# Kernel tuning notes

Measured on AMD Instinct MI355X. Metric: run time of the kernel, lower is better.

The kernel has to match this reference:

```python
import jax, jax.numpy as jnp
import numpy as np

N = 8192          # number of priors
TOP_K = 50        # max detections returned
IOU_THR = 0.3     # NMS IoU threshold (module-level constant)
VAR0, VAR1 = 0.1, 0.2  # variance buffer


def setup_inputs() -> dict:
    key = jax.random.key(0)
    k1, k2, k3, k4, k5 = jax.random.split(key, 5)
    loc = jax.random.normal(k1, (N, 14), jnp.float32)
    conf = jax.random.uniform(k2, (N, 2), jnp.float32)
    # some iou scores slightly out of [0,1] to exercise the clamp
    iou = jax.random.uniform(k3, (N, 1), jnp.float32) * 1.2 - 0.1
    cxcy = jax.random.uniform(k4, (N, 2), jnp.float32)            # anchor centers in [0,1)
    wh = jax.random.uniform(k5, (N, 2), jnp.float32) * 0.19 + 0.01  # anchor sizes in (0.01,0.2)
    priors = jnp.concatenate([cxcy, wh], axis=1)
    return {"loc": loc, "conf": conf, "iou": iou, "priors": priors}


def _decode(loc, conf, iou, priors):
    cls_scores = conf[:, 1]
    iou_scores = jnp.clip(iou[:, 0], 0.0, 1.0)
    scores = jnp.sqrt(cls_scores * iou_scores)
    p_cxcy, p_wh = priors[:, 0:2], priors[:, 2:4]
    bb_cxcy = p_cxcy + loc[:, 0:2] * VAR0 * p_wh
    var = jnp.array([VAR0, VAR1], jnp.float32)
    bb_wh_half = p_wh * jnp.exp(loc[:, 2:4] * var) * 0.5
    bboxes = jnp.concatenate([bb_cxcy - bb_wh_half, bb_cxcy + bb_wh_half], axis=1)
    # 5 landmarks, each decoded like the box center
    lms = jnp.concatenate(
        [p_cxcy + loc[:, 4 + 2 * i:6 + 2 * i] * VAR0 * p_wh for i in range(5)], axis=1)
    return bboxes, lms, scores


def _nms_keep_idx(bboxes, scores):
    """Greedy NMS; returns indices (into original order) of the first TOP_K kept boxes."""
    order = jnp.argsort(-scores)
    b = bboxes[order]
    x1, y1, x2, y2 = b[:, 0], b[:, 1], b[:, 2], b[:, 3]
    area = (x2 - x1) * (y2 - y1)
    iw = jnp.maximum(jnp.minimum(x2[:, None], x2[None, :]) - jnp.maximum(x1[:, None], x1[None, :]), 0.0)
    ih = jnp.maximum(jnp.minimum(y2[:, None], y2[None, :]) - jnp.maximum(y1[:, None], y1[None, :]), 0.0)
    inter = iw * ih
    iou_mat = inter / (area[:, None] + area[None, :] - inter)  # [N, N]
    idxs = jnp.arange(N)

    def body(i, keep):
        suppressed = jnp.any((iou_mat[i] > IOU_THR) & keep & (idxs < i))
        return keep.at[i].set(~suppressed)

    keep = jax.lax.fori_loop(0, N, body, jnp.zeros((N,), bool))
    kept_pos = jnp.nonzero(keep, size=TOP_K, fill_value=0)[0]  # fixed-size under jit
    return order[kept_pos]


def reference(loc, conf, iou, priors):
    bboxes, lms, scores = _decode(loc, conf, iou, priors)
    keep_idx = _nms_keep_idx(bboxes, scores)
    dets = jnp.concatenate(
        [bboxes[keep_idx], lms[keep_idx], scores[keep_idx][:, None]], axis=1)  # [TOP_K, 15]
    return dets
```

## Files before the change

### kernel.cpp

```cpp
#include <hip/hip_runtime.h>

#define NBOX 8192
#define TOP_K 50
#define IOU_THR 0.3f
#define VAR0 0.1f
#define VAR1 0.2f
#define NT 512
#define NWAVE (NT / 64)
#define MSEL 128
#define CAND_MAX 1024
#define BPT 16

__device__ __forceinline__ void decode_box(int cidx, const float* __restrict__ loc,
                                           const float* __restrict__ priors,
                                           float& x1, float& y1, float& x2, float& y2,
                                           float& area)
{
    float4 pr = *reinterpret_cast<const float4*>(priors + 4 * cidx);
    float l0 = loc[cidx * 14 + 0];
    float l1 = loc[cidx * 14 + 1];
    float l2 = loc[cidx * 14 + 2];
    float l3 = loc[cidx * 14 + 3];
    float cx = pr.x + l0 * VAR0 * pr.z;
    float cy = pr.y + l1 * VAR0 * pr.w;
    float hw = pr.z * expf(l2 * VAR0) * 0.5f;
    float hh = pr.w * expf(l3 * VAR1) * 0.5f;
    x1 = cx - hw; y1 = cy - hh; x2 = cx + hw; y2 = cy + hh;
    area = (x2 - x1) * (y2 - y1);
}

__device__ __forceinline__ void find_thresh(unsigned c0, unsigned c1, unsigned c2, unsigned c3,
                                            unsigned base_above, int lane,
                                            int& bin_sel, unsigned& above_sel)
{
    unsigned cnt = c0 + c1 + c2 + c3;
    unsigned S = cnt;
    #pragma unroll
    for (int d = 1; d < 64; d <<= 1) {
        unsigned t = __shfl_down(S, d);
        if (lane + d < 64) S += t;
    }
    unsigned long long bal = __ballot(base_above + S >= MSEL);
    int lstar = 63 - __clzll(bal);
    int src = (lstar < 63) ? (lstar + 1) : lstar;
    unsigned Snext = __shfl(S, src);
    unsigned above = base_above + ((lstar < 63) ? Snext : 0u);
    unsigned bl[4] = {c0, c1, c2, c3};
    int bsel = -1; unsigned abv = above; unsigned acc = above;
    #pragma unroll
    for (int k = 3; k >= 0; --k) {
        if (bsel < 0) {
            if (acc + bl[k] >= MSEL) { bsel = k; abv = acc; }
            else acc += bl[k];
        }
    }
    bin_sel  = 4 * lstar + __shfl(bsel, lstar);
    above_sel = __shfl(abv, lstar);
}

__device__ void bitonic_sort(unsigned long long* a, int S, int tid)
{
    for (int k = 2; k <= S; k <<= 1) {
        for (int j = k >> 1; j > 0; j >>= 1) {
            __syncthreads();
            for (int i = tid; i < S; i += NT) {
                int l = i ^ j;
                if (l > i) {
                    unsigned long long A = a[i];
                    unsigned long long B = a[l];
                    bool asc = ((i & k) == 0);
                    if ((A > B) == asc) { a[i] = B; a[l] = A; }
                }
            }
        }
    }
    __syncthreads();
}

__device__ int greedy_nms_serial(const unsigned long long* __restrict__ arr, int n, int lane,
                                 const float* __restrict__ loc, const float* __restrict__ priors,
                                 int* keep_out)
{
    float kx1 = 0.f, ky1 = 0.f, kx2 = 0.f, ky2 = 0.f, karea = 0.f;
    int my_keep = 0, idx0 = 0, kept = 0;
    bool done = false;
    for (int p = 0; p < n && !done; p += 64) {
        int cidx = 0;
        float x1 = 0.f, y1 = 0.f, x2 = 0.f, y2 = 0.f, area = 0.f;
        int pos = p + lane;
        if (pos < n) {
            cidx = (int)(arr[pos] & 0xFFFFFFFFull);
            decode_box(cidx, loc, priors, x1, y1, x2, y2, area);
        }
        int nb = (n - p) < 64 ? (n - p) : 64;
        for (int c = 0; c < nb; ++c) {
            float bx1 = __shfl(x1, c);
            float by1 = __shfl(y1, c);
            float bx2 = __shfl(x2, c);
            float by2 = __shfl(y2, c);
            float barea = __shfl(area, c);
            int   bidx  = __shfl(cidx, c);
            float iw = fmaxf(fminf(kx2, bx2) - fmaxf(kx1, bx1), 0.0f);
            float ih = fmaxf(fminf(ky2, by2) - fmaxf(ky1, by1), 0.0f);
            float inter = iw * ih;
            float v = inter / (karea + barea - inter);
            bool sup = (lane < kept) && (v > IOU_THR);
            if (__ballot(sup) == 0ull) {
                if (kept == 0) idx0 = bidx;
                if (lane == kept) {
                    kx1 = bx1; ky1 = by1; kx2 = bx2; ky2 = by2; karea = barea;
                    my_keep = bidx;
                }
                ++kept;
                if (kept == TOP_K) { done = true; break; }
            }
        }
    }
    if (lane < TOP_K) keep_out[lane] = (lane < kept) ? my_keep : idx0;
    return kept;
}

__global__ __launch_bounds__(NT) void yunet_fused_kernel(
    const float* __restrict__ loc,
    const float* __restrict__ conf,
    const float* __restrict__ iou,
    const float* __restrict__ priors,
    float* __restrict__ out)
{
    __shared__ unsigned long long keys[NBOX];
    __shared__ unsigned long long cand[CAND_MAX];
    __shared__ unsigned int hist[NWAVE][256];
    __shared__ unsigned int fhist[256];
    __shared__ unsigned long long maskbuf[64];
    __shared__ unsigned long long sh_supprev;
    __shared__ float4 boxb4[64];
    __shared__ float  boxa[64];
    __shared__ float4 keptb4[TOP_K];
    __shared__ float  kepta[TOP_K];
    __shared__ int keep_sh[TOP_K];
    __shared__ unsigned sh_cnt, sh_above, sh_T;
    __shared__ int sh_B, sh_flag, sh_kept;

    const int tid = threadIdx.x;

    {
        unsigned* hz = &hist[0][0];
        for (int i = tid; i < NWAVE * 256; i += NT) hz[i] = 0;
        for (int i = tid; i < 256; i += NT) fhist[i] = 0;
        if (tid == 0) { sh_cnt = 0; sh_flag = 0; sh_kept = 0; }
    }
    __syncthreads();

    unsigned sbv[BPT];
    {
        const float4* conf4 = reinterpret_cast<const float4*>(conf);
        const float4* iou4  = reinterpret_cast<const float4*>(iou);
        float4 cf[8], io[4];
        #pragma unroll
        for (int m = 0; m < 2; ++m)
            #pragma unroll
            for (int q = 0; q < 4; ++q)
                cf[m * 4 + q] = conf4[(m * NT + tid) * 4 + q];
        #pragma unroll
        for (int m = 0; m < 2; ++m)
            #pragma unroll
            for (int r = 0; r < 2; ++r)
                io[m * 2 + r] = iou4[(m * NT + tid) * 2 + r];

        #pragma unroll
        for (int m = 0; m < 2; ++m) {
            float sc[8], uu[8];
            #pragma unroll
            for (int q = 0; q < 4; ++q) {
                sc[2 * q]     = cf[m * 4 + q].y;
                sc[2 * q + 1] = cf[m * 4 + q].w;
            }
            #pragma unroll
            for (int r = 0; r < 2; ++r) {
                uu[4 * r + 0] = io[m * 2 + r].x; uu[4 * r + 1] = io[m * 2 + r].y;
                uu[4 * r + 2] = io[m * 2 + r].z; uu[4 * r + 3] = io[m * 2 + r].w;
            }
            #pragma unroll
            for (int q = 0; q < 8; ++q) {
                float u = fminf(fmaxf(uu[q], 0.0f), 1.0f);
                float s = sqrtf(sc[q] * u);
                unsigned sb = __float_as_uint(s);
                sbv[m * 8 + q] = sb;
                atomicAdd(&hist[tid >> 6][sb >> 24], 1u);
            }
        }
    }
    __syncthreads();

    if (tid < 64) {
        const int lane = tid;
        unsigned c0 = 0, c1 = 0, c2 = 0, c3 = 0;
        #pragma unroll
        for (int w = 0; w < NWAVE; ++w) {
            c0 += hist[w][4 * lane + 0];
            c1 += hist[w][4 * lane + 1];
            c2 += hist[w][4 * lane + 2];
            c3 += hist[w][4 * lane + 3];
        }
        int bs; unsigned ab;
        find_thresh(c0, c1, c2, c3, 0u, lane, bs, ab);
        if (lane == 0) { sh_B = bs; sh_above = ab; }
    }
    __syncthreads();
    const int B = sh_B;
    const unsigned above = sh_above;

    #pragma unroll
    for (int k = 0; k < BPT; ++k) {
        unsigned sb = sbv[k];
        if ((int)(sb >> 24) == B) atomicAdd(&fhist[(sb >> 16) & 255u], 1u);
    }
    __syncthreads();

    if (tid < 64) {
        const int lane = tid;
        int fs; unsigned ab2;
        find_thresh(fhist[4 * lane + 0], fhist[4 * lane + 1],
                    fhist[4 * lane + 2], fhist[4 * lane + 3], above, lane, fs, ab2);
        if (lane == 0) sh_T = ((unsigned)B << 24) | ((unsigned)fs << 16);
    }
    __syncthreads();
    const unsigned T = sh_T;

    #pragma unroll
    for (int m = 0; m < 2; ++m) {
        #pragma unroll
        for (int q = 0; q < 8; ++q) {
            unsigned sb = sbv[m * 8 + q];
            if (sb >= T) {
                unsigned pos = atomicAdd(&sh_cnt, 1u);
                if (pos < CAND_MAX)
                    cand[pos] = ((unsigned long long)(~sb) << 32)
                              | (unsigned)((m * NT + tid) * BPT / 2 + q);
            }
        }
    }
    __syncthreads();
    const int C = (int)sh_cnt;

    if (C <= CAND_MAX) {
        for (int i = tid; i < C; i += NT) {
            unsigned long long k = cand[i];
            int r = 0;
            int j = 0;
            for (; j + 4 <= C; j += 4) {
                r += (cand[j]     < k) ? 1 : 0;
                r += (cand[j + 1] < k) ? 1 : 0;
                r += (cand[j + 2] < k) ? 1 : 0;
                r += (cand[j + 3] < k) ? 1 : 0;
            }
            for (; j < C; ++j) r += (cand[j] < k) ? 1 : 0;
            keys[r] = k;
        }
        __syncthreads();

        for (int p = 0; p < C; p += 64) {
            if (tid < 64) {
                const int lane = tid;
                int pos = p + lane;
                bool valid = pos < C;
                int cidx = valid ? (int)(keys[pos] & 0xFFFFFFFFull) : 0;
                float x1, y1, x2, y2, area;
                decode_box(cidx, loc, priors, x1, y1, x2, y2, area);
                boxb4[lane] = make_float4(x1, y1, x2, y2);
                boxa[lane] = area;
                int kept = sh_kept;
                bool supP = !valid;
                for (int j = 0; j < kept; ++j) {
                    float4 kb = keptb4[j]; float ka = kepta[j];
                    float iw = fmaxf(fminf(x2, kb.z) - fmaxf(x1, kb.x), 0.f);
                    float ih = fmaxf(fminf(y2, kb.w) - fmaxf(y1, kb.y), 0.f);
                    float inter = iw * ih;
                    supP = supP || (inter > IOU_THR * (area + ka - inter));
                }
                unsigned long long sp = __ballot(supP);
                if (lane == 0) sh_supprev = sp;
            }
            __syncthreads();

            {
                int r  = tid >> 3;
                int cb = tid & 7;
                float4 rb = boxb4[r]; float ra = boxa[r];
                unsigned byte = 0;
                #pragma unroll
                for (int k = 0; k < 8; ++k) {
                    int c = cb * 8 + k;
                    float4 cx = boxb4[c]; float ca = boxa[c];
                    float iw = fmaxf(fminf(rb.z, cx.z) - fmaxf(rb.x, cx.x), 0.f);
                    float ih = fmaxf(fminf(rb.w, cx.w) - fmaxf(rb.y, cx.y), 0.f);
                    float inter = iw * ih;
                    byte |= (unsigned)((inter > IOU_THR * (ra + ca - inter)) ? 1u : 0u) << k;
                }
                ((unsigned char*)maskbuf)[tid] = (unsigned char)byte;
            }
            __syncthreads();

            if (tid < 64) {
                const int lane = tid;
                unsigned long long mymask = maskbuf[lane];
                unsigned long long sup_prev = sh_supprev;
                unsigned long long keepcur = 0ull;
                for (int i2 = 0; i2 < 64; ++i2) {
                    unsigned long long mi = __shfl(mymask, i2);
                    unsigned long long lower = (i2 == 0) ? 0ull : (~0ull >> (64 - i2));
                    if (!((sup_prev >> i2) & 1ull) && !(mi & keepcur & lower))
                        keepcur |= (1ull << i2);
                }
                int kept = sh_kept;
                unsigned long long lowm = (lane == 0) ? 0ull : (~0ull >> (64 - lane));
                int rank = kept + __popcll(keepcur & lowm);
                if (((keepcur >> lane) & 1ull) && rank < TOP_K) {
                    keep_sh[rank] = (int)(keys[p + lane] & 0xFFFFFFFFull);
                    keptb4[rank] = boxb4[lane];
                    kepta[rank] = boxa[lane];
                }
                if (lane == 0) sh_kept = kept + __popcll(keepcur);
            }
            __syncthreads();
            if (sh_kept >= TOP_K) break;
        }
        if (tid == 0) sh_flag = (sh_kept >= TOP_K) ? 0 : 1;
    } else {
        if (tid == 0) sh_flag = 1;
    }
    __syncthreads();

    if (sh_flag) {
        #pragma unroll
        for (int m = 0; m < 2; ++m) {
            #pragma unroll
            for (int q = 0; q < 8; ++q) {
                int i = (m * NT + tid) * 8 + q;
                keys[i] = ((unsigned long long)(~sbv[m * 8 + q]) << 32) | (unsigned)i;
            }
        }
        __syncthreads();
        bitonic_sort(keys, NBOX, tid);
        if (tid < 64) greedy_nms_serial(keys, NBOX, tid, loc, priors, keep_sh);
        __syncthreads();
    }

    if (tid < TOP_K) {
        int i = keep_sh[tid];
        float4 pr = *reinterpret_cast<const float4*>(priors + 4 * i);
        float cx = pr.x + loc[i * 14 + 0] * VAR0 * pr.z;
        float cy = pr.y + loc[i * 14 + 1] * VAR0 * pr.w;
        float hw = pr.z * expf(loc[i * 14 + 2] * VAR0) * 0.5f;
        float hh = pr.w * expf(loc[i * 14 + 3] * VAR1) * 0.5f;
        float* o = out + tid * 15;
        o[0] = cx - hw;
        o[1] = cy - hh;
        o[2] = cx + hw;
        o[3] = cy + hh;
        #pragma unroll
        for (int q = 0; q < 5; ++q) {
            o[4 + 2 * q] = pr.x + loc[i * 14 + 4 + 2 * q] * VAR0 * pr.z;
            o[5 + 2 * q] = pr.y + loc[i * 14 + 5 + 2 * q] * VAR0 * pr.w;
        }
        float cc = conf[i * 2 + 1];
        float u  = fminf(fmaxf(iou[i], 0.0f), 1.0f);
        o[14] = sqrtf(cc * u);
    }
}

extern "C" void kernel_launch(void* const* d_in, const int* in_sizes, int n_in,
                              void* d_out, int out_size, void* d_ws, size_t ws_size,
                              hipStream_t stream) {
    const float* loc    = (const float*)d_in[0];
    const float* conf   = (const float*)d_in[1];
    const float* iou    = (const float*)d_in[2];
    const float* priors = (const float*)d_in[3];
    float* out = (float*)d_out;

    yunet_fused_kernel<<<1, NT, 0, stream>>>(loc, conf, iou, priors, out);
}
```

Baseline: 23.27 us.

## Use single-pass linear-bin score histogram and predecode candidate boxes in parallel

After: 23.18 us. Within noise of the previous version (-0.4%).

```diff
diff --git a/kernel.cpp b/kernel.cpp
--- a/kernel.cpp
+++ b/kernel.cpp
@@ -8,7 +8,7 @@
 #define NT 512
 #define NWAVE (NT / 64)
 #define MSEL 128
-#define CAND_MAX 1024
+#define PRE_MAX 256
 #define BPT 16
 
 __device__ __forceinline__ void decode_box(int cidx, const float* __restrict__ loc,
@@ -128,126 +128,102 @@
     float* __restrict__ out)
 {
     __shared__ unsigned long long keys[NBOX];
-    __shared__ unsigned long long cand[CAND_MAX];
-    __shared__ unsigned int hist[NWAVE][256];
-    __shared__ unsigned int fhist[256];
+    __shared__ unsigned long long cand[PRE_MAX];
+    __shared__ unsigned hist[NWAVE][256] __attribute__((aligned(16)));
     __shared__ unsigned long long maskbuf[64];
     __shared__ unsigned long long sh_supprev;
-    __shared__ float4 boxb4[64];
-    __shared__ float  boxa[64];
+    __shared__ float4 boxs4[PRE_MAX];
+    __shared__ float  boxsa[PRE_MAX];
     __shared__ float4 keptb4[TOP_K];
     __shared__ float  kepta[TOP_K];
     __shared__ int keep_sh[TOP_K];
-    __shared__ unsigned sh_cnt, sh_above, sh_T;
-    __shared__ int sh_B, sh_flag, sh_kept;
+    __shared__ unsigned sh_cnt;
+    __shared__ int sh_flag, sh_kept;
 
     const int tid = threadIdx.x;
+    const int lane = tid & 63;
+
+    const float4* conf4 = reinterpret_cast<const float4*>(conf);
+    const float4* iou4  = reinterpret_cast<const float4*>(iou);
+    float4 cf[8], io[4];
+    #pragma unroll
+    for (int m = 0; m < 2; ++m)
+        #pragma unroll
+        for (int q = 0; q < 4; ++q)
+            cf[m * 4 + q] = conf4[(m * NT + tid) * 4 + q];
+    #pragma unroll
+    for (int m = 0; m < 2; ++m)
+        #pragma unroll
+        for (int r = 0; r < 2; ++r)
+            io[m * 2 + r] = iou4[(m * NT + tid) * 2 + r];
 
     {
         unsigned* hz = &hist[0][0];
         for (int i = tid; i < NWAVE * 256; i += NT) hz[i] = 0;
-        for (int i = tid; i < 256; i += NT) fhist[i] = 0;
         if (tid == 0) { sh_cnt = 0; sh_flag = 0; sh_kept = 0; }
     }
     __syncthreads();
 
     unsigned sbv[BPT];
+    #pragma unroll
+    for (int m = 0; m < 2; ++m) {
+        float sc[8], uu[8];
+        #pragma unroll
+        for (int q = 0; q < 4; ++q) {
+            sc[2 * q]     = cf[m * 4 + q].y;
+            sc[2 * q + 1] = cf[m * 4 + q].w;
+        }
+        #pragma unroll
+        for (int r = 0; r < 2; ++r) {
+            uu[4 * r + 0] = io[m * 2 + r].x; uu[4 * r + 1] = io[m * 2 + r].y;
+            uu[4 * r + 2] = io[m * 2 + r].z; uu[4 * r + 3] = io[m * 2 + r].w;
+        }
+        #pragma unroll
+        for (int q = 0; q < 8; ++q) {
+            float u = fminf(fmaxf(uu[q], 0.0f), 1.0f);
+            float s = sqrtf(sc[q] * u);
+            unsigned sb = __float_as_uint(s);
+            sbv[m * 8 + q] = sb;
+            int bin = (int)(s * 256.0f); bin = bin > 255 ? 255 : bin;
+            atomicAdd(&hist[tid >> 6][bin], 1u);
+        }
+    }
+    __syncthreads();
+
+    int B;
     {
-        const float4* conf4 = reinterpret_cast<const float4*>(conf);
-        const float4* iou4  = reinterpret_cast<const float4*>(iou);
-        float4 cf[8], io[4];
-        #pragma unroll
-        for (int m = 0; m < 2; ++m)
-            #pragma unroll
-            for (int q = 0; q < 4; ++q)
-                cf[m * 4 + q] = conf4[(m * NT + tid) * 4 + q];
-        #pragma unroll
-        for (int m = 0; m < 2; ++m)
-            #pragma unroll
-            for (int r = 0; r < 2; ++r)
-                io[m * 2 + r] = iou4[(m * NT + tid) * 2 + r];
-
-        #pragma unroll
-        for (int m = 0; m < 2; ++m) {
-            float sc[8], uu[8];
-            #pragma unroll
-            for (int q = 0; q < 4; ++q) {
-                sc[2 * q]     = cf[m * 4 + q].y;
-                sc[2 * q + 1] = cf[m * 4 + q].w;
-            }
-            #pragma unroll
-            for (int r = 0; r < 2; ++r) {
-                uu[4 * r + 0] = io[m * 2 + r].x; uu[4 * r + 1] = io[m * 2 + r].y;
-                uu[4 * r + 2] = io[m * 2 + r].z; uu[4 * r + 3] = io[m * 2 + r].w;
-            }
-            #pragma unroll
-            for (int q = 0; q < 8; ++q) {
-                float u = fminf(fmaxf(uu[q], 0.0f), 1.0f);
-                float s = sqrtf(sc[q] * u);
-                unsigned sb = __float_as_uint(s);
-                sbv[m * 8 + q] = sb;
-                atomicAdd(&hist[tid >> 6][sb >> 24], 1u);
-            }
-        }
-    }
-    __syncthreads();
-
-    if (tid < 64) {
-        const int lane = tid;
         unsigned c0 = 0, c1 = 0, c2 = 0, c3 = 0;
         #pragma unroll
         for (int w = 0; w < NWAVE; ++w) {
-            c0 += hist[w][4 * lane + 0];
-            c1 += hist[w][4 * lane + 1];
-            c2 += hist[w][4 * lane + 2];
-            c3 += hist[w][4 * lane + 3];
-        }
-        int bs; unsigned ab;
-        find_thresh(c0, c1, c2, c3, 0u, lane, bs, ab);
-        if (lane == 0) { sh_B = bs; sh_above = ab; }
-    }
-    __syncthreads();
-    const int B = sh_B;
-    const unsigned above = sh_above;
-
-    #pragma unroll
-    for (int k = 0; k < BPT; ++k) {
-        unsigned sb = sbv[k];
-        if ((int)(sb >> 24) == B) atomicAdd(&fhist[(sb >> 16) & 255u], 1u);
-    }
-    __syncthreads();
-
-    if (tid < 64) {
-        const int lane = tid;
-        int fs; unsigned ab2;
-        find_thresh(fhist[4 * lane + 0], fhist[4 * lane + 1],
-                    fhist[4 * lane + 2], fhist[4 * lane + 3], above, lane, fs, ab2);
-        if (lane == 0) sh_T = ((unsigned)B << 24) | ((unsigned)fs << 16);
-    }
-    __syncthreads();
-    const unsigned T = sh_T;
+            uint4 h = *(const uint4*)&hist[w][4 * lane];
+            c0 += h.x; c1 += h.y; c2 += h.z; c3 += h.w;
+        }
+        unsigned ab;
+        find_thresh(c0, c1, c2, c3, 0u, lane, B, ab);
+    }
 
     #pragma unroll
     for (int m = 0; m < 2; ++m) {
         #pragma unroll
         for (int q = 0; q < 8; ++q) {
             unsigned sb = sbv[m * 8 + q];
-            if (sb >= T) {
+            float s = __uint_as_float(sb);
+            int bin = (int)(s * 256.0f); bin = bin > 255 ? 255 : bin;
+            if (bin >= B) {
                 unsigned pos = atomicAdd(&sh_cnt, 1u);
-                if (pos < CAND_MAX)
+                if (pos < PRE_MAX)
                     cand[pos] = ((unsigned long long)(~sb) << 32)
-                              | (unsigned)((m * NT + tid) * BPT / 2 + q);
+                              | (unsigned)((m * NT + tid) * 8 + q);
             }
         }
     }
     __syncthreads();
     const int C = (int)sh_cnt;
 
-    if (C <= CAND_MAX) {
-        for (int i = tid; i < C; i += NT) {
-            unsigned long long k = cand[i];
-            int r = 0;
-            int j = 0;
+    if (C <= PRE_MAX) {
+        if (tid < C) {
+            unsigned long long k = cand[tid];
+            int r = 0, j = 0;
             for (; j + 4 <= C; j += 4) {
                 r += (cand[j]     < k) ? 1 : 0;
                 r += (cand[j + 1] < k) ? 1 : 0;
@@ -256,27 +232,28 @@
             }
             for (; j < C; ++j) r += (cand[j] < k) ? 1 : 0;
             keys[r] = k;
+            int cidx = (int)(k & 0xFFFFFFFFull);
+            float x1, y1, x2, y2, area;
+            decode_box(cidx, loc, priors, x1, y1, x2, y2, area);
+            boxs4[r] = make_float4(x1, y1, x2, y2);
+            boxsa[r] = area;
         }
         __syncthreads();
 
         for (int p = 0; p < C; p += 64) {
             if (tid < 64) {
-                const int lane = tid;
                 int pos = p + lane;
                 bool valid = pos < C;
-                int cidx = valid ? (int)(keys[pos] & 0xFFFFFFFFull) : 0;
-                float x1, y1, x2, y2, area;
-                decode_box(cidx, loc, priors, x1, y1, x2, y2, area);
-                boxb4[lane] = make_float4(x1, y1, x2, y2);
-                boxa[lane] = area;
+                int rp = valid ? pos : 0;
+                float4 b = boxs4[rp]; float a = boxsa[rp];
                 int kept = sh_kept;
                 bool supP = !valid;
                 for (int j = 0; j < kept; ++j) {
                     float4 kb = keptb4[j]; float ka = kepta[j];
-                    float iw = fmaxf(fminf(x2, kb.z) - fmaxf(x1, kb.x), 0.f);
-                    float ih = fmaxf(fminf(y2, kb.w) - fmaxf(y1, kb.y), 0.f);
+                    float iw = fmaxf(fminf(b.z, kb.z) - fmaxf(b.x, kb.x), 0.f);
+                    float ih = fmaxf(fminf(b.w, kb.w) - fmaxf(b.y, kb.y), 0.f);
                     float inter = iw * ih;
-                    supP = supP || (inter > IOU_THR * (area + ka - inter));
+                    supP = supP || (inter > IOU_THR * (a + ka - inter));
                 }
                 unsigned long long sp = __ballot(supP);
                 if (lane == 0) sh_supprev = sp;
@@ -286,12 +263,14 @@
             {
                 int r  = tid >> 3;
                 int cb = tid & 7;
-                float4 rb = boxb4[r]; float ra = boxa[r];
+                int rp = (p + r < C) ? p + r : 0;
+                float4 rb = boxs4[rp]; float ra = boxsa[rp];
                 unsigned byte = 0;
                 #pragma unroll
                 for (int k = 0; k < 8; ++k) {
                     int c = cb * 8 + k;
-                    float4 cx = boxb4[c]; float ca = boxa[c];
+                    int cp = (p + c < C) ? p + c : 0;
+                    float4 cx = boxs4[cp]; float ca = boxsa[cp];
                     float iw = fmaxf(fminf(rb.z, cx.z) - fmaxf(rb.x, cx.x), 0.f);
                     float ih = fmaxf(fminf(rb.w, cx.w) - fmaxf(rb.y, cx.y), 0.f);
                     float inter = iw * ih;
@@ -302,25 +281,28 @@
             __syncthreads();
 
             if (tid < 64) {
-                const int lane = tid;
                 unsigned long long mymask = maskbuf[lane];
                 unsigned long long sup_prev = sh_supprev;
                 unsigned long long keepcur = 0ull;
-                for (int i2 = 0; i2 < 64; ++i2) {
+                const int kept0 = sh_kept;
+                int kept = kept0;
+                for (int i2 = 0; i2 < 64 && kept < TOP_K; ++i2) {
                     unsigned long long mi = __shfl(mymask, i2);
-                    unsigned long long lower = (i2 == 0) ? 0ull : (~0ull >> (64 - i2));
-                    if (!((sup_prev >> i2) & 1ull) && !(mi & keepcur & lower))
-                        keepcur |= (1ull << i2);
-                }
-                int kept = sh_kept;
-                unsigned long long lowm = (lane == 0) ? 0ull : (~0ull >> (64 - lane));
-                int rank = kept + __popcll(keepcur & lowm);
+                    unsigned long long lower = (1ull << i2) - 1ull;
+                    if (!((sup_prev >> i2) & 1ull) && !(mi & keepcur & lower)) {
+                        keepcur |= 1ull << i2;
+                        ++kept;
+                    }
+                }
+                unsigned long long lowm = (1ull << lane) - 1ull;
+                int rank = kept0 + __popcll(keepcur & lowm);
                 if (((keepcur >> lane) & 1ull) && rank < TOP_K) {
-                    keep_sh[rank] = (int)(keys[p + lane] & 0xFFFFFFFFull);
-                    keptb4[rank] = boxb4[lane];
-                    kepta[rank] = boxa[lane];
-                }
-                if (lane == 0) sh_kept = kept + __popcll(keepcur);
+                    int pos = p + lane;
+                    keep_sh[rank] = (int)(keys[pos] & 0xFFFFFFFFull);
+                    keptb4[rank] = boxs4[pos];
+                    kepta[rank] = boxsa[pos];
+                }
+                if (lane == 0) sh_kept = kept;
             }
             __syncthreads();
             if (sh_kept >= TOP_K) break;
@@ -343,11 +325,13 @@
         __syncthreads();
         bitonic_sort(keys, NBOX, tid);
         if (tid < 64) greedy_nms_serial(keys, NBOX, tid, loc, priors, keep_sh);
+        if (tid == 0) sh_kept = TOP_K;
         __syncthreads();
     }
 
     if (tid < TOP_K) {
-        int i = keep_sh[tid];
+        int src = (tid < sh_kept) ? tid : 0;
+        int i = keep_sh[src];
         float4 pr = *reinterpret_cast<const float4*>(priors + 4 * i);
         float cx = pr.x + loc[i * 14 + 0] * VAR0 * pr.z;
         float cy = pr.y + loc[i * 14 + 1] * VAR0 * pr.w;
```
